# Kernel tuning notes

Measured on AMD Instinct MI355X. Metric: run time of the kernel, lower is better.

The kernel has to match this reference:

```python
import jax, jax.numpy as jnp
import numpy as np

BN_EPS = 1e-5

def _bn(h, gamma, beta, mean, var):
    # inference-mode BatchNorm1d
    return (h - mean) * jax.lax.rsqrt(var + BN_EPS) * gamma + beta


def setup_inputs() -> dict:
    key = jax.random.key(0)
    ks = jax.random.split(key, 16)
    N, E, D_in, D, L = 100000, 640000, 256, 128, 3
    s = 0.05
    return {
        "x": jax.random.normal(ks[0], (N, D_in), jnp.float32),
        "edge_index": jax.random.randint(ks[1], (2, E), 0, N, jnp.int32),
        "W_in": jax.random.normal(ks[2], (D_in, D), jnp.float32) * s,
        "b_in": jax.random.normal(ks[3], (D,), jnp.float32) * s,
        "bn_in_gamma": jax.random.uniform(ks[4], (D,), jnp.float32, 0.5, 1.5),
        "bn_in_beta": jax.random.normal(ks[5], (D,), jnp.float32) * s,
        "bn_in_mean": jax.random.normal(ks[6], (D,), jnp.float32) * s,
        "bn_in_var": jax.random.uniform(ks[7], (D,), jnp.float32, 0.5, 1.5),
        "Wl": jax.random.normal(ks[8], (L, D, D), jnp.float32) * s,
        "bl": jax.random.normal(ks[9], (L, D), jnp.float32) * s,
        "Wr": jax.random.normal(ks[10], (L, D, D), jnp.float32) * s,
        "bn_gamma": jax.random.uniform(ks[11], (L, D), jnp.float32, 0.5, 1.5),
        "bn_beta": jax.random.normal(ks[12], (L, D), jnp.float32) * s,
        "bn_mean": jax.random.normal(ks[13], (L, D), jnp.float32) * s,
        "bn_var": jax.random.uniform(ks[14], (L, D), jnp.float32, 0.5, 1.5),
    }


def reference(x, edge_index, W_in, b_in, bn_in_gamma, bn_in_beta, bn_in_mean,
              bn_in_var, Wl, bl, Wr, bn_gamma, bn_beta, bn_mean, bn_var):
    N = x.shape[0]
    src, dst = edge_index[0], edge_index[1]
    # in-degree (clamped to 1 so isolated nodes aggregate to 0, matching PyG mean)
    deg = jax.ops.segment_sum(jnp.ones_like(dst, jnp.float32), dst, num_segments=N)
    deg = jnp.maximum(deg, 1.0)[:, None]  # [N, 1]

    # input projection + BN + ReLU (dropout = identity in eval)
    h = jax.nn.relu(_bn(x @ W_in + b_in, bn_in_gamma, bn_in_beta, bn_in_mean, bn_in_var))

    L = Wl.shape[0]
    for l in range(L):
        # SAGEConv(mean): lin_l(mean_j h_j) + lin_r(h_i)
        agg = jax.ops.segment_sum(h[src], dst, num_segments=N) / deg  # [N, D]
        h_new = agg @ Wl[l] + bl[l] + h @ Wr[l]
        h_new = jax.nn.relu(_bn(h_new, bn_gamma[l], bn_beta[l], bn_mean[l], bn_var[l]))
        h = h + h_new  # residual
    return h
```

## Files before the change

kernel.cpp:

```cpp
#include <hip/hip_runtime.h>

#define BN_EPS 1e-5f

typedef __bf16 bf16x8 __attribute__((ext_vector_type(8)));
typedef float f32x4 __attribute__((ext_vector_type(4)));
typedef unsigned int uint;
typedef unsigned short ushort;

__device__ __forceinline__ ushort f2bf(float f) {
  union { float f; uint u; } v; v.f = f;
  uint r = v.u + 0x7FFF + ((v.u >> 16) & 1);
  return (ushort)(r >> 16);
}
__device__ __forceinline__ float bf2f_lo(uint u) {
  union { uint i; float f; } v; v.i = u << 16; return v.f;
}
__device__ __forceinline__ float bf2f_hi(uint u) {
  union { uint i; float f; } v; v.i = u & 0xffff0000u; return v.f;
}
__device__ __forceinline__ uint pack2(float a, float b) {
  return (uint)f2bf(a) | ((uint)f2bf(b) << 16);
}


__global__ void hist_kernel(const int* __restrict__ dst, int* __restrict__ cnt, int E) {
  int e = blockIdx.x * 256 + threadIdx.x;
  if (e < E) atomicAdd(&cnt[dst[e]], 1);
}

__device__ __forceinline__ int block_exscan256(int v, int tid, int* ws4) {
  __syncthreads();
  int lane = tid & 63, w = tid >> 6;
  int x = v;
  #pragma unroll
  for (int off = 1; off < 64; off <<= 1) {
    int y = __shfl_up(x, off, 64);
    if (lane >= off) x += y;
  }
  if (lane == 63) ws4[w] = x;
  __syncthreads();
  if (tid == 0) {
    int s = 0;
    for (int i = 0; i < 4; ++i) { int t = ws4[i]; ws4[i] = s; s += t; }
  }
  __syncthreads();
  return ws4[w] + x - v;
}

__global__ void blocksum_kernel(const int* __restrict__ cnt, int* __restrict__ bsum, int N) {
  __shared__ int ws4[4];
  int tid = threadIdx.x;
  int i = blockIdx.x * 256 + tid;
  int v = (i < N) ? cnt[i] : 0;
  #pragma unroll
  for (int off = 32; off > 0; off >>= 1) v += __shfl_down(v, off, 64);
  if ((tid & 63) == 0) ws4[tid >> 6] = v;
  __syncthreads();
  if (tid == 0) bsum[blockIdx.x] = ws4[0] + ws4[1] + ws4[2] + ws4[3];
}

__global__ void scanbsum_kernel(const int* __restrict__ bsum, int* __restrict__ boff,
                                int NB, int* __restrict__ rowptr, int N, int E) {
  __shared__ int ws4[4];
  __shared__ int tot;
  int tid = threadIdx.x;
  int carry = 0;
  for (int base = 0; base < NB; base += 256) {
    int i = base + tid;
    int v = (i < NB) ? bsum[i] : 0;
    int ex = block_exscan256(v, tid, ws4);
    if (i < NB) boff[i] = carry + ex;
    if (tid == 255) tot = ex + v;
    __syncthreads();
    carry += tot;
  }
  if (tid == 0) rowptr[N] = E;
}

__global__ void writerowptr_kernel(const int* __restrict__ cnt, const int* __restrict__ boff,
                                   int* __restrict__ rowptr, int N) {
  __shared__ int ws4[4];
  int tid = threadIdx.x;
  int i = blockIdx.x * 256 + tid;
  int v = (i < N) ? cnt[i] : 0;
  int ex = block_exscan256(v, tid, ws4);
  if (i < N) rowptr[i] = boff[blockIdx.x] + ex;
}

__global__ void fill_kernel(const int* __restrict__ src, const int* __restrict__ dst,
                            const int* __restrict__ rowptr, int* __restrict__ cur,
                            int* __restrict__ col, int E) {
  int e = blockIdx.x * 256 + threadIdx.x;
  if (e < E) {
    int d = dst[e];
    int p = rowptr[d] + atomicAdd(&cur[d], 1);
    col[p] = src[e];
  }
}

__global__ void deginv_kernel(const int* __restrict__ rowptr, float* __restrict__ dinv, int N) {
  int i = blockIdx.x * 256 + threadIdx.x;
  if (i < N) {
    int d = rowptr[i + 1] - rowptr[i];
    dinv[i] = 1.0f / (float)(d > 0 ? d : 1);
  }
}


__global__ void prep_weights_fm(const float* __restrict__ W_in, const float* __restrict__ Wl,
                                const float* __restrict__ Wr, ushort* __restrict__ Bfm) {
  int p = blockIdx.x * 256 + threadIdx.x;
  int mat = p >> 12, rem = p & 4095;
  int nt = rem >> 9, kt = (rem >> 6) & 7, lane = rem & 63;
  int n = nt * 16 + (lane & 15);
  int k0 = kt * 32 + (lane >> 4) * 8;
  ushort tmp[8];
  #pragma unroll
  for (int j = 0; j < 8; ++j) {
    int k = k0 + j;
    float v;
    if (mat == 0) v = W_in[k * 128 + n];
    else {
      int l = mat - 1;
      v = (k < 128) ? Wl[l * 16384 + k * 128 + n] : Wr[l * 16384 + (k - 128) * 128 + n];
    }
    tmp[j] = f2bf(v);
  }
  *(uint4*)&Bfm[(size_t)p * 8] = *(const uint4*)tmp;
}


__global__ void agg_kernel(const int* __restrict__ rowptr, const int* __restrict__ col,
                           const float* __restrict__ dinv, const ushort* __restrict__ h,
                           ushort* __restrict__ agg, int N) {
  int node = blockIdx.x * 4 + (threadIdx.x >> 6);
  if (node >= N) return;
  int lane = threadIdx.x & 63;
  int beg = rowptr[node], end = rowptr[node + 1];
  float ax = 0.f, ay = 0.f;
  int e = beg;
  for (; e + 3 < end; e += 4) {
    int s0 = col[e], s1 = col[e + 1], s2 = col[e + 2], s3 = col[e + 3];
    uint v0 = *(const uint*)(h + (size_t)s0 * 128 + lane * 2);
    uint v1 = *(const uint*)(h + (size_t)s1 * 128 + lane * 2);
    uint v2 = *(const uint*)(h + (size_t)s2 * 128 + lane * 2);
    uint v3 = *(const uint*)(h + (size_t)s3 * 128 + lane * 2);
    ax += (bf2f_lo(v0) + bf2f_lo(v1)) + (bf2f_lo(v2) + bf2f_lo(v3));
    ay += (bf2f_hi(v0) + bf2f_hi(v1)) + (bf2f_hi(v2) + bf2f_hi(v3));
  }
  for (; e < end; ++e) {
    uint v0 = *(const uint*)(h + (size_t)col[e] * 128 + lane * 2);
    ax += bf2f_lo(v0);
    ay += bf2f_hi(v0);
  }
  float di = dinv[node];
  *(uint*)(agg + (size_t)node * 128 + lane * 2) = pack2(ax * di, ay * di);
}


template<bool F32OUT>
__global__ __launch_bounds__(256, 2)
void gemm_layer(const ushort* __restrict__ A0, const ushort* __restrict__ A1,
                const ushort* __restrict__ Bfm, const float* __restrict__ bias,
                const float* __restrict__ gamma, const float* __restrict__ beta,
                const float* __restrict__ mean, const float* __restrict__ var,
                const ushort* __restrict__ residual, void* __restrict__ out, int N) {
  __shared__ ushort Bs[32768];
  int tid = threadIdx.x, wave = tid >> 6, lane = tid & 63;
  int wm = wave >> 1, wn = wave & 1, quad = lane >> 4, l16 = lane & 15;
  int m0 = blockIdx.x * 128;

  int rowm[4];
  #pragma unroll
  for (int mt = 0; mt < 4; ++mt) {
    int r = m0 + wm * 64 + mt * 16 + l16;
    rowm[mt] = r < N ? r : N - 1;
  }

  uint4 a_buf[2][4];
  {
    const ushort* bse = A0;
    int ko = quad * 8;
    #pragma unroll
    for (int mt = 0; mt < 4; ++mt)
      a_buf[0][mt] = *(const uint4*)(bse + (size_t)rowm[mt] * 128 + ko);
  }

  #pragma unroll
  for (int i = 0; i < 16; ++i) {
    int idx = i * 256 + tid;
    *(uint4*)&Bs[(size_t)idx * 8] = *(const uint4*)&Bfm[(size_t)idx * 8];
  }
  __syncthreads();

  f32x4 acc[4][4] = {};

  #pragma unroll
  for (int kt = 0; kt < 8; ++kt) {
    if (kt < 7) {
      const ushort* bse = (kt + 1 < 4) ? A0 : A1;
      int ko = ((kt + 1) & 3) * 32 + quad * 8;
      #pragma unroll
      for (int mt = 0; mt < 4; ++mt)
        a_buf[(kt + 1) & 1][mt] = *(const uint4*)(bse + (size_t)rowm[mt] * 128 + ko);
    }
    bf16x8 bfr[4];
    #pragma unroll
    for (int nt = 0; nt < 4; ++nt)
      bfr[nt] = *(bf16x8*)&Bs[((size_t)((wn * 4 + nt) * 8 + kt) * 64 + lane) * 8];
    #pragma unroll
    for (int mt = 0; mt < 4; ++mt) {
      bf16x8 af = __builtin_bit_cast(bf16x8, a_buf[kt & 1][mt]);
      #pragma unroll
      for (int nt = 0; nt < 4; ++nt)
        acc[mt][nt] = __builtin_amdgcn_mfma_f32_16x16x32_bf16(af, bfr[nt], acc[mt][nt], 0, 0, 0);
    }
  }

  #pragma unroll
  for (int nt = 0; nt < 4; ++nt) {
    int c = wn * 64 + nt * 16 + l16;
    float sc = gamma[c] * rsqrtf(var[c] + BN_EPS);
    float sh = beta[c] - mean[c] * sc;
    float bi = bias[c];
    #pragma unroll
    for (int mt = 0; mt < 4; ++mt)
      #pragma unroll
      for (int r = 0; r < 4; ++r)
        acc[mt][nt][r] = fmaxf((acc[mt][nt][r] + bi) * sc + sh, 0.f);
  }

  __syncthreads();
  float* Cb = (float*)Bs + wave * (16 * 68);
  #pragma unroll
  for (int mt = 0; mt < 4; ++mt) {
    #pragma unroll
    for (int nt = 0; nt < 4; ++nt)
      #pragma unroll
      for (int r = 0; r < 4; ++r)
        Cb[(quad * 4 + r) * 68 + nt * 16 + l16] = acc[mt][nt][r];
    #pragma unroll
    for (int i = 0; i < 4; ++i) {
      int idx = i * 64 + lane, rowl = idx >> 4, seg = idx & 15;
      int grow = m0 + wm * 64 + mt * 16 + rowl;
      if (grow < N) {
        float4 vv = *(float4*)&Cb[rowl * 68 + seg * 4];
        uint2 rv = *(const uint2*)(residual + (size_t)grow * 128 + wn * 64 + seg * 4);
        vv.x += bf2f_lo(rv.x); vv.y += bf2f_hi(rv.x);
        vv.z += bf2f_lo(rv.y); vv.w += bf2f_hi(rv.y);
        if (F32OUT) {
          *(float4*)((float*)out + (size_t)grow * 128 + wn * 64 + seg * 4) = vv;
        } else {
          uint2 o;
          o.x = pack2(vv.x, vv.y); o.y = pack2(vv.z, vv.w);
          *(uint2*)((ushort*)out + (size_t)grow * 128 + wn * 64 + seg * 4) = o;
        }
      }
    }
  }
}


__global__ __launch_bounds__(256, 2)
void gemm_in(const float* __restrict__ X, const ushort* __restrict__ Bfm,
             const float* __restrict__ bias,
             const float* __restrict__ gamma, const float* __restrict__ beta,
             const float* __restrict__ mean, const float* __restrict__ var,
             ushort* __restrict__ out, int N) {
  __shared__ ushort Bs[32768];
  int tid = threadIdx.x, wave = tid >> 6, lane = tid & 63;
  int wm = wave >> 1, wn = wave & 1, quad = lane >> 4, l16 = lane & 15;
  int m0 = blockIdx.x * 128;

  int rowm[4];
  #pragma unroll
  for (int mt = 0; mt < 4; ++mt) {
    int r = m0 + wm * 64 + mt * 16 + l16;
    rowm[mt] = r < N ? r : N - 1;
  }

  float4 f_buf[2][4][2];
  {
    int ko = quad * 8;
    #pragma unroll
    for (int mt = 0; mt < 4; ++mt) {
      const float* p = X + (size_t)rowm[mt] * 256 + ko;
      f_buf[0][mt][0] = *(const float4*)p;
      f_buf[0][mt][1] = *(const float4*)(p + 4);
    }
  }

  #pragma unroll
  for (int i = 0; i < 16; ++i) {
    int idx = i * 256 + tid;
    *(uint4*)&Bs[(size_t)idx * 8] = *(const uint4*)&Bfm[(size_t)idx * 8];
  }
  __syncthreads();

  f32x4 acc[4][4] = {};

  #pragma unroll
  for (int kt = 0; kt < 8; ++kt) {
    if (kt < 7) {
      int ko = (kt + 1) * 32 + quad * 8;
      #pragma unroll
      for (int mt = 0; mt < 4; ++mt) {
        const float* p = X + (size_t)rowm[mt] * 256 + ko;
        f_buf[(kt + 1) & 1][mt][0] = *(const float4*)p;
        f_buf[(kt + 1) & 1][mt][1] = *(const float4*)(p + 4);
      }
    }
    bf16x8 bfr[4];
    #pragma unroll
    for (int nt = 0; nt < 4; ++nt)
      bfr[nt] = *(bf16x8*)&Bs[((size_t)((wn * 4 + nt) * 8 + kt) * 64 + lane) * 8];
    #pragma unroll
    for (int mt = 0; mt < 4; ++mt) {
      float4 lo = f_buf[kt & 1][mt][0], hi = f_buf[kt & 1][mt][1];
      uint4 av;
      av.x = pack2(lo.x, lo.y); av.y = pack2(lo.z, lo.w);
      av.z = pack2(hi.x, hi.y); av.w = pack2(hi.z, hi.w);
      bf16x8 af = __builtin_bit_cast(bf16x8, av);
      #pragma unroll
      for (int nt = 0; nt < 4; ++nt)
        acc[mt][nt] = __builtin_amdgcn_mfma_f32_16x16x32_bf16(af, bfr[nt], acc[mt][nt], 0, 0, 0);
    }
  }

  #pragma unroll
  for (int nt = 0; nt < 4; ++nt) {
    int c = wn * 64 + nt * 16 + l16;
    float sc = gamma[c] * rsqrtf(var[c] + BN_EPS);
    float sh = beta[c] - mean[c] * sc;
    float bi = bias[c];
    #pragma unroll
    for (int mt = 0; mt < 4; ++mt)
      #pragma unroll
      for (int r = 0; r < 4; ++r)
        acc[mt][nt][r] = fmaxf((acc[mt][nt][r] + bi) * sc + sh, 0.f);
  }

  __syncthreads();
  float* Cb = (float*)Bs + wave * (16 * 68);
  #pragma unroll
  for (int mt = 0; mt < 4; ++mt) {
    #pragma unroll
    for (int nt = 0; nt < 4; ++nt)
      #pragma unroll
      for (int r = 0; r < 4; ++r)
        Cb[(quad * 4 + r) * 68 + nt * 16 + l16] = acc[mt][nt][r];
    #pragma unroll
    for (int i = 0; i < 4; ++i) {
      int idx = i * 64 + lane, rowl = idx >> 4, seg = idx & 15;
      int grow = m0 + wm * 64 + mt * 16 + rowl;
      if (grow < N) {
        float4 vv = *(float4*)&Cb[rowl * 68 + seg * 4];
        uint2 o;
        o.x = pack2(vv.x, vv.y); o.y = pack2(vv.z, vv.w);
        *(uint2*)(out + (size_t)grow * 128 + wn * 64 + seg * 4) = o;
      }
    }
  }
}


extern "C" void kernel_launch(void* const* d_in, const int* in_sizes, int n_in,
                              void* d_out, int out_size, void* d_ws, size_t ws_size,
                              hipStream_t stream) {
  const float* x      = (const float*)d_in[0];
  const int*   eidx   = (const int*)d_in[1];
  const float* W_in   = (const float*)d_in[2];
  const float* b_in   = (const float*)d_in[3];
  const float* bng_in = (const float*)d_in[4];
  const float* bnb_in = (const float*)d_in[5];
  const float* bnm_in = (const float*)d_in[6];
  const float* bnv_in = (const float*)d_in[7];
  const float* Wl     = (const float*)d_in[8];
  const float* bl     = (const float*)d_in[9];
  const float* Wr     = (const float*)d_in[10];
  const float* bng    = (const float*)d_in[11];
  const float* bnb    = (const float*)d_in[12];
  const float* bnm    = (const float*)d_in[13];
  const float* bnv    = (const float*)d_in[14];

  const int N = in_sizes[0] / 256;
  const int E = in_sizes[1] / 2;
  const int NB = (N + 255) / 256;
  const int* src = eidx;
  const int* dst = eidx + E;

  char* ws = (char*)d_ws;
  size_t off = 0;
  auto alloc = [&](size_t bytes) {
    void* p = ws + off;
    off = (off + bytes + 255) & ~(size_t)255;
    return p;
  };
  int* cnt      = (int*)alloc((size_t)N * 4);
  int* rowptr   = (int*)alloc((size_t)(N + 1) * 4);
  int* bsum     = (int*)alloc((size_t)NB * 4);
  int* boff     = (int*)alloc((size_t)NB * 4);
  int* col      = (int*)alloc((size_t)E * 4);
  float* dinv   = (float*)alloc((size_t)N * 4);
  ushort* Bfm   = (ushort*)alloc(4 * 32768 * 2);
  ushort* hA    = (ushort*)alloc((size_t)N * 128 * 2);
  ushort* hB    = (ushort*)alloc((size_t)N * 128 * 2);
  ushort* agg   = (ushort*)alloc((size_t)N * 128 * 2);
  (void)ws_size; (void)n_in; (void)out_size;

  const int EB = (E + 255) / 256;
  const int GB = (N + 127) / 128;

  hipMemsetAsync(cnt, 0, (size_t)N * 4, stream);
  hist_kernel<<<EB, 256, 0, stream>>>(dst, cnt, E);
  blocksum_kernel<<<NB, 256, 0, stream>>>(cnt, bsum, N);
  scanbsum_kernel<<<1, 256, 0, stream>>>(bsum, boff, NB, rowptr, N, E);
  writerowptr_kernel<<<NB, 256, 0, stream>>>(cnt, boff, rowptr, N);
  hipMemsetAsync(cnt, 0, (size_t)N * 4, stream);
  fill_kernel<<<EB, 256, 0, stream>>>(src, dst, rowptr, cnt, col, E);
  deginv_kernel<<<NB, 256, 0, stream>>>(rowptr, dinv, N);

  prep_weights_fm<<<64, 256, 0, stream>>>(W_in, Wl, Wr, Bfm);

  gemm_in<<<GB, 256, 0, stream>>>(x, Bfm, b_in, bng_in, bnb_in, bnm_in, bnv_in, hA, N);

  ushort* hbuf[2] = { hA, hB };
  for (int l = 0; l < 3; ++l) {
    const ushort* h_in = hbuf[l & 1];
    agg_kernel<<<(N + 3) / 4, 256, 0, stream>>>(rowptr, col, dinv, h_in, agg, N);
    const ushort* BfmL = Bfm + (size_t)(l + 1) * 32768;
    const float* biasL = bl + l * 128;
    if (l < 2) {
      gemm_layer<false><<<GB, 256, 0, stream>>>(agg, h_in, BfmL, biasL,
          bng + l * 128, bnb + l * 128, bnm + l * 128, bnv + l * 128,
          h_in, (void*)hbuf[(l + 1) & 1], N);
    } else {
      gemm_layer<true><<<GB, 256, 0, stream>>>(agg, h_in, BfmL, biasL,
          bng + l * 128, bnb + l * 128, bnm + l * 128, bnv + l * 128,
          h_in, d_out, N);
    }
  }
}
```

Measured before the change: 503.4 us.

## Halve GEMM weight LDS footprint via two-phase staging; narrow aggregation to 32 lanes per node

The GEMM kernels now hold only half of the 128x256 bf16 weight tile in LDS at a time. They reload the second half mid-loop behind barriers, and the weight prep kernel reorders the layout so each half is contiguous. This cuts LDS per block so three blocks can be resident per CU instead of two, at the cost of an extra barrier and a reload in the middle of the K loop. Separately, the aggregation kernel now uses 32 lanes per node with 8-byte loads, handling 8 nodes per block, to widen memory transactions in the gather. A custom barrier that waits only on LDS counters replaces __syncthreads.

```diff
diff --git a/kernel.cpp b/kernel.cpp
--- a/kernel.cpp
+++ b/kernel.cpp
@@ -20,6 +20,13 @@
 }
 __device__ __forceinline__ uint pack2(float a, float b) {
   return (uint)f2bf(a) | ((uint)f2bf(b) << 16);
+}
+
+__device__ __forceinline__ void lds_barrier() {
+  asm volatile("" ::: "memory");
+  __builtin_amdgcn_s_waitcnt(0xC07F);
+  __builtin_amdgcn_s_barrier();
+  asm volatile("" ::: "memory");
 }
 
 
@@ -110,10 +117,13 @@
 __global__ void prep_weights_fm(const float* __restrict__ W_in, const float* __restrict__ Wl,
                                 const float* __restrict__ Wr, ushort* __restrict__ Bfm) {
   int p = blockIdx.x * 256 + threadIdx.x;
-  int mat = p >> 12, rem = p & 4095;
-  int nt = rem >> 9, kt = (rem >> 6) & 7, lane = rem & 63;
+  int mat = p >> 12;
+  int rem = p & 4095;
+  int half = rem >> 11;
+  int rem2 = rem & 2047;
+  int nt = rem2 >> 8, kt2 = (rem2 >> 6) & 3, lane = rem2 & 63;
   int n = nt * 16 + (lane & 15);
-  int k0 = kt * 32 + (lane >> 4) * 8;
+  int k0 = (half * 4 + kt2) * 32 + (lane >> 4) * 8;
   ushort tmp[8];
   #pragma unroll
   for (int j = 0; j < 8; ++j) {
@@ -133,39 +143,44 @@
 __global__ void agg_kernel(const int* __restrict__ rowptr, const int* __restrict__ col,
                            const float* __restrict__ dinv, const ushort* __restrict__ h,
                            ushort* __restrict__ agg, int N) {
-  int node = blockIdx.x * 4 + (threadIdx.x >> 6);
+  int node = blockIdx.x * 8 + (threadIdx.x >> 5);
   if (node >= N) return;
-  int lane = threadIdx.x & 63;
+  int lane = threadIdx.x & 31;
+  const ushort* hp = h + lane * 4;
   int beg = rowptr[node], end = rowptr[node + 1];
-  float ax = 0.f, ay = 0.f;
+  float a0 = 0.f, a1 = 0.f, a2 = 0.f, a3 = 0.f;
   int e = beg;
   for (; e + 3 < end; e += 4) {
-    int s0 = col[e], s1 = col[e + 1], s2 = col[e + 2], s3 = col[e + 3];
-    uint v0 = *(const uint*)(h + (size_t)s0 * 128 + lane * 2);
-    uint v1 = *(const uint*)(h + (size_t)s1 * 128 + lane * 2);
-    uint v2 = *(const uint*)(h + (size_t)s2 * 128 + lane * 2);
-    uint v3 = *(const uint*)(h + (size_t)s3 * 128 + lane * 2);
-    ax += (bf2f_lo(v0) + bf2f_lo(v1)) + (bf2f_lo(v2) + bf2f_lo(v3));
-    ay += (bf2f_hi(v0) + bf2f_hi(v1)) + (bf2f_hi(v2) + bf2f_hi(v3));
+    uint2 v0 = *(const uint2*)(hp + (size_t)col[e] * 128);
+    uint2 v1 = *(const uint2*)(hp + (size_t)col[e + 1] * 128);
+    uint2 v2 = *(const uint2*)(hp + (size_t)col[e + 2] * 128);
+    uint2 v3 = *(const uint2*)(hp + (size_t)col[e + 3] * 128);
+    a0 += (bf2f_lo(v0.x) + bf2f_lo(v1.x)) + (bf2f_lo(v2.x) + bf2f_lo(v3.x));
+    a1 += (bf2f_hi(v0.x) + bf2f_hi(v1.x)) + (bf2f_hi(v2.x) + bf2f_hi(v3.x));
+    a2 += (bf2f_lo(v0.y) + bf2f_lo(v1.y)) + (bf2f_lo(v2.y) + bf2f_lo(v3.y));
+    a3 += (bf2f_hi(v0.y) + bf2f_hi(v1.y)) + (bf2f_hi(v2.y) + bf2f_hi(v3.y));
   }
   for (; e < end; ++e) {
-    uint v0 = *(const uint*)(h + (size_t)col[e] * 128 + lane * 2);
-    ax += bf2f_lo(v0);
-    ay += bf2f_hi(v0);
+    uint2 v0 = *(const uint2*)(hp + (size_t)col[e] * 128);
+    a0 += bf2f_lo(v0.x); a1 += bf2f_hi(v0.x);
+    a2 += bf2f_lo(v0.y); a3 += bf2f_hi(v0.y);
   }
   float di = dinv[node];
-  *(uint*)(agg + (size_t)node * 128 + lane * 2) = pack2(ax * di, ay * di);
+  uint2 o;
+  o.x = pack2(a0 * di, a1 * di);
+  o.y = pack2(a2 * di, a3 * di);
+  *(uint2*)(agg + (size_t)node * 128 + lane * 4) = o;
 }
 
 
 template<bool F32OUT>
-__global__ __launch_bounds__(256, 2)
+__global__ __launch_bounds__(256, 3)
 void gemm_layer(const ushort* __restrict__ A0, const ushort* __restrict__ A1,
                 const ushort* __restrict__ Bfm, const float* __restrict__ bias,
                 const float* __restrict__ gamma, const float* __restrict__ beta,
                 const float* __restrict__ mean, const float* __restrict__ var,
                 const ushort* __restrict__ residual, void* __restrict__ out, int N) {
-  __shared__ ushort Bs[32768];
+  __shared__ ushort Bs[16384];
   int tid = threadIdx.x, wave = tid >> 6, lane = tid & 63;
   int wm = wave >> 1, wn = wave & 1, quad = lane >> 4, l16 = lane & 15;
   int m0 = blockIdx.x * 128;
@@ -178,42 +193,51 @@
   }
 
   uint4 a_buf[2][4];
-  {
-    const ushort* bse = A0;
-    int ko = quad * 8;
-    #pragma unroll
-    for (int mt = 0; mt < 4; ++mt)
-      a_buf[0][mt] = *(const uint4*)(bse + (size_t)rowm[mt] * 128 + ko);
-  }
-
-  #pragma unroll
-  for (int i = 0; i < 16; ++i) {
+  #pragma unroll
+  for (int mt = 0; mt < 4; ++mt)
+    a_buf[0][mt] = *(const uint4*)(A0 + (size_t)rowm[mt] * 128 + quad * 8);
+
+  #pragma unroll
+  for (int i = 0; i < 8; ++i) {
     int idx = i * 256 + tid;
-    *(uint4*)&Bs[(size_t)idx * 8] = *(const uint4*)&Bfm[(size_t)idx * 8];
-  }
-  __syncthreads();
+    *(uint4*)&Bs[idx * 8] = *(const uint4*)&Bfm[idx * 8];
+  }
+  lds_barrier();
 
   f32x4 acc[4][4] = {};
 
   #pragma unroll
-  for (int kt = 0; kt < 8; ++kt) {
-    if (kt < 7) {
-      const ushort* bse = (kt + 1 < 4) ? A0 : A1;
-      int ko = ((kt + 1) & 3) * 32 + quad * 8;
-      #pragma unroll
-      for (int mt = 0; mt < 4; ++mt)
-        a_buf[(kt + 1) & 1][mt] = *(const uint4*)(bse + (size_t)rowm[mt] * 128 + ko);
-    }
-    bf16x8 bfr[4];
-    #pragma unroll
-    for (int nt = 0; nt < 4; ++nt)
-      bfr[nt] = *(bf16x8*)&Bs[((size_t)((wn * 4 + nt) * 8 + kt) * 64 + lane) * 8];
-    #pragma unroll
-    for (int mt = 0; mt < 4; ++mt) {
-      bf16x8 af = __builtin_bit_cast(bf16x8, a_buf[kt & 1][mt]);
+  for (int h = 0; h < 2; ++h) {
+    #pragma unroll
+    for (int k2 = 0; k2 < 4; ++k2) {
+      int kt = h * 4 + k2;
+      if (kt < 7) {
+        const ushort* bse = (kt + 1 < 4) ? A0 : A1;
+        int ko = ((kt + 1) & 3) * 32 + quad * 8;
+        #pragma unroll
+        for (int mt = 0; mt < 4; ++mt)
+          a_buf[(kt + 1) & 1][mt] = *(const uint4*)(bse + (size_t)rowm[mt] * 128 + ko);
+      }
+      bf16x8 bfr[4];
       #pragma unroll
       for (int nt = 0; nt < 4; ++nt)
-        acc[mt][nt] = __builtin_amdgcn_mfma_f32_16x16x32_bf16(af, bfr[nt], acc[mt][nt], 0, 0, 0);
+        bfr[nt] = *(bf16x8*)&Bs[(((wn * 4 + nt) * 4 + k2) * 64 + lane) * 8];
+      #pragma unroll
+      for (int mt = 0; mt < 4; ++mt) {
+        bf16x8 af = __builtin_bit_cast(bf16x8, a_buf[kt & 1][mt]);
+        #pragma unroll
+        for (int nt = 0; nt < 4; ++nt)
+          acc[mt][nt] = __builtin_amdgcn_mfma_f32_16x16x32_bf16(af, bfr[nt], acc[mt][nt], 0, 0, 0);
+      }
+    }
+    if (h == 0) {
+      lds_barrier();
+      #pragma unroll
+      for (int i = 0; i < 8; ++i) {
+        int idx = i * 256 + tid;
+        *(uint4*)&Bs[idx * 8] = *(const uint4*)&Bfm[16384 + idx * 8];
+      }
+      lds_barrier();
     }
   }
 
@@ -230,7 +254,7 @@
         acc[mt][nt][r] = fmaxf((acc[mt][nt][r] + bi) * sc + sh, 0.f);
   }
 
-  __syncthreads();
+  lds_barrier();
   float* Cb = (float*)Bs + wave * (16 * 68);
   #pragma unroll
   for (int mt = 0; mt < 4; ++mt) {
@@ -261,13 +285,13 @@
 }
 
 
-__global__ __launch_bounds__(256, 2)
+__global__ __launch_bounds__(256, 3)
 void gemm_in(const float* __restrict__ X, const ushort* __restrict__ Bfm,
              const float* __restrict__ bias,
              const float* __restrict__ gamma, const float* __restrict__ beta,
              const float* __restrict__ mean, const float* __restrict__ var,
              ushort* __restrict__ out, int N) {
-  __shared__ ushort Bs[32768];
+  __shared__ ushort Bs[16384];
   int tid = threadIdx.x, wave = tid >> 6, lane = tid & 63;
   int wm = wave >> 1, wn = wave & 1, quad = lane >> 4, l16 = lane & 15;
   int m0 = blockIdx.x * 128;
@@ -280,50 +304,60 @@
   }
 
   float4 f_buf[2][4][2];
-  {
-    int ko = quad * 8;
-    #pragma unroll
-    for (int mt = 0; mt < 4; ++mt) {
-      const float* p = X + (size_t)rowm[mt] * 256 + ko;
-      f_buf[0][mt][0] = *(const float4*)p;
-      f_buf[0][mt][1] = *(const float4*)(p + 4);
-    }
-  }
-
-  #pragma unroll
-  for (int i = 0; i < 16; ++i) {
+  #pragma unroll
+  for (int mt = 0; mt < 4; ++mt) {
+    const float* p = X + (size_t)rowm[mt] * 256 + quad * 8;
+    f_buf[0][mt][0] = *(const float4*)p;
+    f_buf[0][mt][1] = *(const float4*)(p + 4);
+  }
+
+  #pragma unroll
+  for (int i = 0; i < 8; ++i) {
     int idx = i * 256 + tid;
-    *(uint4*)&Bs[(size_t)idx * 8] = *(const uint4*)&Bfm[(size_t)idx * 8];
-  }
-  __syncthreads();
+    *(uint4*)&Bs[idx * 8] = *(const uint4*)&Bfm[idx * 8];
+  }
+  lds_barrier();
 
   f32x4 acc[4][4] = {};
 
   #pragma unroll
-  for (int kt = 0; kt < 8; ++kt) {
-    if (kt < 7) {
-      int ko = (kt + 1) * 32 + quad * 8;
+  for (int h = 0; h < 2; ++h) {
+    #pragma unroll
+    for (int k2 = 0; k2 < 4; ++k2) {
+      int kt = h * 4 + k2;
+      if (kt < 7) {
+        int ko = (kt + 1) * 32 + quad * 8;
+        #pragma unroll
+        for (int mt = 0; mt < 4; ++mt) {
+          const float* p = X + (size_t)rowm[mt] * 256 + ko;
+          f_buf[(kt + 1) & 1][mt][0] = *(const float4*)p;
+          f_buf[(kt + 1) & 1][mt][1] = *(const float4*)(p + 4);
+        }
+      }
+      bf16x8 bfr[4];
+      #pragma unroll
+      for (int nt = 0; nt < 4; ++nt)
+        bfr[nt] = *(bf16x8*)&Bs[(((wn * 4 + nt) * 4 + k2) * 64 + lane) * 8];
       #pragma unroll
       for (int mt = 0; mt < 4; ++mt) {
-        const float* p = X + (size_t)rowm[mt] * 256 + ko;
-        f_buf[(kt + 1) & 1][mt][0] = *(const float4*)p;
-        f_buf[(kt + 1) & 1][mt][1] = *(const float4*)(p + 4);
-      }
-    }
-    bf16x8 bfr[4];
-    #pragma unroll
-    for (int nt = 0; nt < 4; ++nt)
-      bfr[nt] = *(bf16x8*)&Bs[((size_t)((wn * 4 + nt) * 8 + kt) * 64 + lane) * 8];
-    #pragma unroll
-    for (int mt = 0; mt < 4; ++mt) {
-      float4 lo = f_buf[kt & 1][mt][0], hi = f_buf[kt & 1][mt][1];
-      uint4 av;
-      av.x = pack2(lo.x, lo.y); av.y = pack2(lo.z, lo.w);
-      av.z = pack2(hi.x, hi.y); av.w = pack2(hi.z, hi.w);
-      bf16x8 af = __builtin_bit_cast(bf16x8, av);
-      #pragma unroll
-      for (int nt = 0; nt < 4; ++nt)
-        acc[mt][nt] = __builtin_amdgcn_mfma_f32_16x16x32_bf16(af, bfr[nt], acc[mt][nt], 0, 0, 0);
+        float4 lo = f_buf[kt & 1][mt][0], hi = f_buf[kt & 1][mt][1];
+        uint4 av;
+        av.x = pack2(lo.x, lo.y); av.y = pack2(lo.z, lo.w);
+        av.z = pack2(hi.x, hi.y); av.w = pack2(hi.z, hi.w);
+        bf16x8 af = __builtin_bit_cast(bf16x8, av);
+        #pragma unroll
+        for (int nt = 0; nt < 4; ++nt)
+          acc[mt][nt] = __builtin_amdgcn_mfma_f32_16x16x32_bf16(af, bfr[nt], acc[mt][nt], 0, 0, 0);
+      }
+    }
+    if (h == 0) {
+      lds_barrier();
+      #pragma unroll
+      for (int i = 0; i < 8; ++i) {
+        int idx = i * 256 + tid;
+        *(uint4*)&Bs[idx * 8] = *(const uint4*)&Bfm[16384 + idx * 8];
+      }
+      lds_barrier();
     }
   }
 
@@ -340,7 +374,7 @@
         acc[mt][nt][r] = fmaxf((acc[mt][nt][r] + bi) * sc + sh, 0.f);
   }
 
-  __syncthreads();
+  lds_barrier();
   float* Cb = (float*)Bs + wave * (16 * 68);
   #pragma unroll
   for (int mt = 0; mt < 4; ++mt) {
@@ -427,7 +461,7 @@
   ushort* hbuf[2] = { hA, hB };
   for (int l = 0; l < 3; ++l) {
     const ushort* h_in = hbuf[l & 1];
-    agg_kernel<<<(N + 3) / 4, 256, 0, stream>>>(rowptr, col, dinv, h_in, agg, N);
+    agg_kernel<<<(N + 7) / 8, 256, 0, stream>>>(rowptr, col, dinv, h_in, agg, N);
     const ushort* BfmL = Bfm + (size_t)(l + 1) * 32768;
     const float* biasL = bl + l * 128;
     if (l < 2) {
```

Measured after the change: 490.8 us. -2.5%, faster.
